# Performance work log

Measured on AMD Instinct MI355X. Metric: run time of the kernel, lower is better.

Reference implementation:

```python
import jax, jax.numpy as jnp
import numpy as np

G = 8192          # graphs per hand side (PyG batch)
J_SRC = 17        # source-hand joints (transform: Linear(17*64, 13*64))
J_TGT = 13        # target-hand joints
NEG_SLOPE = 0.01  # F.leaky_relu default


def _chain_edge_index(J, num_graphs):
    # bidirectional chain tree per graph, block-diagonal batched like PyG
    p = np.arange(J - 1); c = np.arange(1, J)
    src = np.concatenate([p, c]); dst = np.concatenate([c, p])
    base = np.arange(num_graphs)[:, None] * J
    return jnp.asarray(np.stack([(src[None] + base).ravel(), (dst[None] + base).ravel()]), jnp.int32)


def _lin_init(key, o, i):
    k1, k2 = jax.random.split(key)
    s = 1.0 / np.sqrt(i)
    return (jax.random.uniform(k1, (o, i), jnp.float32, -s, s),
            jax.random.uniform(k2, (o,), jnp.float32, -s, s))


def setup_inputs() -> dict:
    key = jax.random.key(0)
    ks = iter(jax.random.split(key, 64))
    inp = {}
    Nl = G * J_SRC
    inp["l_hand_x"] = jax.random.normal(next(ks), (Nl, 3), jnp.float32)
    inp["r_hand_x"] = jax.random.normal(next(ks), (Nl, 3), jnp.float32)
    ei_src = _chain_edge_index(J_SRC, G)
    inp["l_hand_edge_index"] = ei_src
    inp["r_hand_edge_index"] = ei_src
    E_src = ei_src.shape[1]
    inp["l_hand_edge_attr"] = jax.random.normal(next(ks), (E_src, 3), jnp.float32)
    inp["r_hand_edge_attr"] = jax.random.normal(next(ks), (E_src, 3), jnp.float32)
    ei_t = _chain_edge_index(J_TGT, G)
    inp["hand_edge_index"] = ei_t
    inp["hand_edge_attr"] = jax.random.normal(next(ks), (ei_t.shape[1], 6), jnp.float32)
    Nt = G * J_TGT
    inp["hand_lower"] = -(jax.random.uniform(next(ks), (Nt, 1), jnp.float32) + 0.5)
    inp["hand_upper"] = jax.random.uniform(next(ks), (Nt, 1), jnp.float32) + 0.5
    inp["hand_offset"] = jax.random.normal(next(ks), (Nt, 3), jnp.float32) * 0.05
    ax = jax.random.normal(next(ks), (Nt, 3), jnp.float32)
    inp["hand_axis"] = ax / jnp.linalg.norm(ax, axis=-1, keepdims=True)
    par = np.concatenate([[-1], np.arange(J_TGT - 1)])  # chain: root then parents
    inp["hand_parent"] = jnp.asarray(np.tile(par, G), jnp.int32)
    inp["num_graphs"] = G
    dims = {"enc1_lin": (16, 9),  "enc1_up": (16, 3),
            "enc2_lin": (32, 35), "enc2_up": (32, 16),
            "enc3_lin": (64, 67), "enc3_up": (64, 32),
            "trans":    (13 * 64, 17 * 64),
            "dec1_lin": (32, 138), "dec1_up": (32, 66),
            "dec2_lin": (16, 70),  "dec2_up": (16, 32),
            "dec3_lin": (1, 38),   "dec3_up": (1, 16)}
    for n, (o, i) in dims.items():
        W, b = _lin_init(next(ks), o, i)
        inp[n + "_W"] = W; inp[n + "_b"] = b
    return inp


def _block(x, ei, ea, Wl, bl, Wu, bu):
    # SpatialBasicBlock: gather x_i/x_j, concat edge_attr, linear+leaky_relu,
    # scatter-add at target nodes, residual upsample of x.
    src, dst = ei[0], ei[1]
    z = jnp.concatenate([x[dst], x[src], ea], axis=-1)  # [E, 2*in+edge]
    m = jax.nn.leaky_relu(z @ Wl.T + bl, NEG_SLOPE)
    agg = jax.ops.segment_sum(m, dst, num_segments=x.shape[0])
    return agg + x @ Wu.T + bu


def _rodrigues(ax, ang):
    # rotation matrices about unit axis ax [...,3] by angle ang [...]
    c = jnp.cos(ang)[..., None, None]; s = jnp.sin(ang)[..., None, None]
    I = jnp.eye(3, dtype=ax.dtype)
    aa = ax[..., :, None] * ax[..., None, :]
    x, y, z = ax[..., 0], ax[..., 1], ax[..., 2]
    zero = jnp.zeros_like(x)
    K = jnp.stack([jnp.stack([zero, -z, y], -1),
                   jnp.stack([z, zero, -x], -1),
                   jnp.stack([-y, x, zero], -1)], -2)
    return c * I + (1 - c) * aa + s * K


def _fk(ang, parent, offset, axis, num_graphs, J):
    # forward kinematics along parent chain (parent[j] < j, root = -1)
    a = ang.reshape(num_graphs, J)
    off = offset.reshape(num_graphs, J, 3)
    ax = axis.reshape(num_graphs, J, 3)
    par = parent.reshape(num_graphs, J)[0]  # same topology in every graph
    Rl = _rodrigues(ax, a)                  # [G, J, 3, 3] local rotations
    I = jnp.eye(3, dtype=ang.dtype)
    pos = jnp.zeros((num_graphs, J, 3), ang.dtype)
    rot = jnp.zeros((num_graphs, J, 3, 3), ang.dtype)
    for j in range(J):  # J=13 fixed structural loop
        p = par[j]
        root = p < 0
        Rp = jnp.where(root, I, jnp.take(rot, p, axis=1))
        Pp = jnp.where(root, 0.0, jnp.take(pos, p, axis=1))
        pos = pos.at[:, j].set(Pp + jnp.einsum('gab,gb->ga', Rp, off[:, j]))
        rot = rot.at[:, j].set(jnp.einsum('gab,gbc->gac', Rp, Rl[:, j]))
    return pos.reshape(-1, 3)


def reference(l_hand_x, r_hand_x, l_hand_edge_index, r_hand_edge_index,
              l_hand_edge_attr, r_hand_edge_attr, hand_edge_index, hand_edge_attr,
              hand_lower, hand_upper, hand_offset, hand_axis, hand_parent, num_graphs,
              enc1_lin_W, enc1_lin_b, enc1_up_W, enc1_up_b,
              enc2_lin_W, enc2_lin_b, enc2_up_W, enc2_up_b,
              enc3_lin_W, enc3_lin_b, enc3_up_W, enc3_up_b,
              trans_W, trans_b,
              dec1_lin_W, dec1_lin_b, dec1_up_W, dec1_up_b,
              dec2_lin_W, dec2_lin_b, dec2_up_W, dec2_up_b,
              dec3_lin_W, dec3_lin_b, dec3_up_W, dec3_up_b):
    # ---- encode ----
    Nl = l_hand_x.shape[0]
    x = jnp.concatenate([l_hand_x, r_hand_x], axis=0)
    ei = jnp.concatenate([l_hand_edge_index, r_hand_edge_index + Nl], axis=1)
    ea = jnp.concatenate([l_hand_edge_attr, r_hand_edge_attr], axis=0)
    h = _block(x, ei, ea, enc1_lin_W, enc1_lin_b, enc1_up_W, enc1_up_b)
    h = _block(h, ei, ea, enc2_lin_W, enc2_lin_b, enc2_up_W, enc2_up_b)
    h = _block(h, ei, ea, enc3_lin_W, enc3_lin_b, enc3_up_W, enc3_up_b)
    G2 = 2 * num_graphs
    z = jnp.tanh(h.reshape(G2, -1) @ trans_W.T + trans_b).reshape(-1, 64)
    # ---- decode ----
    half = z.shape[0] // 2
    ei_t = jnp.concatenate([hand_edge_index, hand_edge_index + half], axis=1)
    ea_t = jnp.concatenate([hand_edge_attr, hand_edge_attr], axis=0)
    lower = jnp.concatenate([hand_lower, hand_lower], axis=0)
    upper = jnp.concatenate([hand_upper, hand_upper], axis=0)
    offset = jnp.concatenate([hand_offset, hand_offset], axis=0)
    axis = jnp.concatenate([hand_axis, hand_axis], axis=0)
    parent = jnp.concatenate([hand_parent, hand_parent], axis=0)
    xd = jnp.concatenate([z, lower, upper], axis=1)  # [2*G*13, 66]
    h = _block(xd, ei_t, ea_t, dec1_lin_W, dec1_lin_b, dec1_up_W, dec1_up_b)
    h = _block(h, ei_t, ea_t, dec2_lin_W, dec2_lin_b, dec2_up_W, dec2_up_b)
    ang = jnp.tanh(_block(h, ei_t, ea_t, dec3_lin_W, dec3_lin_b, dec3_up_W, dec3_up_b))
    ang = lower + (upper - lower) * (ang + 1) / 2
    pos = _fk(ang, parent, offset, axis, G2, J_TGT)
    hn = ang.shape[0] // 2
    return ang[:hn], pos[:hn], ang[hn:], pos[hn:]
```

## Files before the change

### kernel.cpp

```cpp
#include <hip/hip_runtime.h>
#include <math.h>


constexpr int G_NUM = 8192;
constexpr int JS = 17;
constexpr int JT = 13;
constexpr int N_ENC = 2 * G_NUM * JS;
constexpr int N_DEC = 2 * G_NUM * JT;
constexpr int G2 = 2 * G_NUM;
constexpr int HN = G_NUM * JT;
constexpr int K_TR = JS * 64;
constexpr int N_TR = JT * 64;

typedef unsigned short u16;
typedef u16   u16x8 __attribute__((ext_vector_type(8)));
typedef u16   u16x4 __attribute__((ext_vector_type(4)));
typedef float f32x4 __attribute__((ext_vector_type(4)));
typedef __bf16 bf16x8 __attribute__((ext_vector_type(8)));

__device__ __forceinline__ float lrelu(float v) { return v > 0.f ? v : 0.01f * v; }
__device__ __forceinline__ u16 f2bf(float f) {
    unsigned u = __float_as_uint(f);
    u += 0x7fff + ((u >> 16) & 1);
    return (u16)(u >> 16);
}
__device__ __forceinline__ float bf2f(u16 h) { return __uint_as_float((unsigned)h << 16); }

template<int K_MM, int C_IN_W, int C_OUT, int C_E, int J, int G, bool TAIL>
__global__ __launch_bounds__(256)
void block_mfma(const u16* __restrict__ xHi, const u16* __restrict__ xLo,
                const float* __restrict__ eaA, const float* __restrict__ eaB, int g_half,
                const float* __restrict__ lowv, const float* __restrict__ upv,
                const float* __restrict__ Wl, const float* __restrict__ bl,
                const float* __restrict__ Wu, const float* __restrict__ bu,
                u16* __restrict__ outHi, u16* __restrict__ outLo)
{
    constexpr int ROWS = G * J;
    constexpr int F = (ROWS + 15) / 16;
    constexpr int NCH = C_OUT / 16;
    constexpr int KF = K_MM / 32;
    constexpr int KPAD = K_MM + 8;
    constexpr int EAS = 2 * (J - 1) * C_E;
    constexpr int CTOT = 2 * C_IN_W + C_E;
    constexpr int CW = (C_IN_W < K_MM) ? C_IN_W : K_MM;
    constexpr int WGG = 4 * G;

    __shared__ __align__(16) u16 sWH[3 * C_OUT * KPAD], sWL[3 * C_OUT * KPAD];
    __shared__ float sEA[WGG * EAS];
    __shared__ float sWe[C_OUT * C_E];
    __shared__ float sBl[C_OUT], sBu[C_OUT];
    __shared__ float sTl[TAIL ? 6 * C_OUT : 1];
    __shared__ float sLow[TAIL ? WGG * J : 1], sUpp[TAIL ? WGG * J : 1];

    const int t = threadIdx.x;
    const int g0 = blockIdx.x * WGG;

    for (int i = t; i < 3 * C_OUT * K_MM; i += 256) {
        const int ch = i / K_MM, k = i % K_MM;
        const int p = ch / C_OUT, o = ch % C_OUT;
        float v = 0.f;
        if (k < CW) {
            if (p == 0)      v = Wl[o * CTOT + k];
            else if (p == 1) v = Wl[o * CTOT + C_IN_W + k];
            else             v = Wu[o * C_IN_W + k];
        }
        const u16 h = f2bf(v);
        sWH[ch * KPAD + k] = h;
        sWL[ch * KPAD + k] = f2bf(v - bf2f(h));
    }
    for (int i = t; i < WGG * EAS; i += 256) {
        const int lg = i / EAS, r = i % EAS;
        const int g = g0 + lg;
        sEA[i] = (g < g_half) ? eaA[(size_t)g * EAS + r]
                              : eaB[(size_t)(g - g_half) * EAS + r];
    }
    for (int i = t; i < C_OUT * C_E; i += 256)
        sWe[i] = Wl[(i / C_E) * CTOT + 2 * C_IN_W + (i % C_E)];
    if (t < C_OUT) { sBl[t] = bl[t]; sBu[t] = bu[t]; }
    if constexpr (TAIL) {
        if (t < C_OUT) {
            sTl[t * 6 + 0] = Wl[t * CTOT + K_MM];
            sTl[t * 6 + 1] = Wl[t * CTOT + K_MM + 1];
            sTl[t * 6 + 2] = Wl[t * CTOT + C_IN_W + K_MM];
            sTl[t * 6 + 3] = Wl[t * CTOT + C_IN_W + K_MM + 1];
            sTl[t * 6 + 4] = Wu[t * C_IN_W + K_MM];
            sTl[t * 6 + 5] = Wu[t * C_IN_W + K_MM + 1];
        }
        for (int i = t; i < WGG * J; i += 256) {
            const int lg = i / J, j = i % J;
            const int g = g0 + lg;
            const int ge = (g < g_half) ? g : g - g_half;
            sLow[i] = lowv[ge * J + j];
            sUpp[i] = upv[ge * J + j];
        }
    }
    __syncthreads();

    const int wv = t >> 6, lane = t & 63;
    const int col = lane & 15, kg = lane >> 4;
    const size_t baseNode = (size_t)(blockIdx.x * 4 + wv) * ROWS;
    const int lgB = wv * G;

    for (int ch = 0; ch < NCH; ++ch) {
        const int o = ch * 16 + col;
        bf16x8 wUh[KF], wUl[KF], wVh[KF], wVl[KF], wPh[KF], wPl[KF];
        #pragma unroll
        for (int kf = 0; kf < KF; ++kf) {
            wUh[kf] = *(const bf16x8*)&sWH[(0 * C_OUT + o) * KPAD + kf * 32 + kg * 8];
            wUl[kf] = *(const bf16x8*)&sWL[(0 * C_OUT + o) * KPAD + kf * 32 + kg * 8];
            wVh[kf] = *(const bf16x8*)&sWH[(1 * C_OUT + o) * KPAD + kf * 32 + kg * 8];
            wVl[kf] = *(const bf16x8*)&sWL[(1 * C_OUT + o) * KPAD + kf * 32 + kg * 8];
            wPh[kf] = *(const bf16x8*)&sWH[(2 * C_OUT + o) * KPAD + kf * 32 + kg * 8];
            wPl[kf] = *(const bf16x8*)&sWL[(2 * C_OUT + o) * KPAD + kf * 32 + kg * 8];
        }
        float we[C_E];
        #pragma unroll
        for (int k = 0; k < C_E; ++k) we[k] = sWe[o * C_E + k];
        const float blo = sBl[o], buo = sBu[o];
        float tl0 = 0, tl1 = 0, tl2 = 0, tl3 = 0, tl4 = 0, tl5 = 0;
        if constexpr (TAIL) {
            tl0 = sTl[o * 6 + 0]; tl1 = sTl[o * 6 + 1]; tl2 = sTl[o * 6 + 2];
            tl3 = sTl[o * 6 + 3]; tl4 = sTl[o * 6 + 4]; tl5 = sTl[o * 6 + 5];
        }

        f32x4 Vpp = {0,0,0,0}, Vp = {0,0,0,0};
        f32x4 Up = {0,0,0,0}, Pp = {0,0,0,0};
        #pragma unroll
        for (int f = 0; f <= F; ++f) {
            f32x4 Vc = {0,0,0,0}, Uc = {0,0,0,0}, Pc = {0,0,0,0};
            if (f < F) {
                const int nrow = f * 16 + col;
                const size_t nd = baseNode + (nrow < ROWS ? nrow : ROWS - 1);
                #pragma unroll
                for (int kf = 0; kf < KF; ++kf) {
                    const bf16x8 aH = *(const bf16x8*)&xHi[nd * K_MM + kf * 32 + kg * 8];
                    const bf16x8 aL = *(const bf16x8*)&xLo[nd * K_MM + kf * 32 + kg * 8];
                    Vc = __builtin_amdgcn_mfma_f32_16x16x32_bf16(aH, wVh[kf], Vc, 0, 0, 0);
                    Vc = __builtin_amdgcn_mfma_f32_16x16x32_bf16(aH, wVl[kf], Vc, 0, 0, 0);
                    Vc = __builtin_amdgcn_mfma_f32_16x16x32_bf16(aL, wVh[kf], Vc, 0, 0, 0);
                    Uc = __builtin_amdgcn_mfma_f32_16x16x32_bf16(aH, wUh[kf], Uc, 0, 0, 0);
                    Uc = __builtin_amdgcn_mfma_f32_16x16x32_bf16(aH, wUl[kf], Uc, 0, 0, 0);
                    Uc = __builtin_amdgcn_mfma_f32_16x16x32_bf16(aL, wUh[kf], Uc, 0, 0, 0);
                    Pc = __builtin_amdgcn_mfma_f32_16x16x32_bf16(aH, wPh[kf], Pc, 0, 0, 0);
                    Pc = __builtin_amdgcn_mfma_f32_16x16x32_bf16(aH, wPl[kf], Pc, 0, 0, 0);
                    Pc = __builtin_amdgcn_mfma_f32_16x16x32_bf16(aL, wPh[kf], Pc, 0, 0, 0);
                }
            }
            if (f >= 1) {
                const int fm = f - 1;
                const float vL0a = __shfl(Vpp[3], 48 + col);
                const float vL0b = __shfl(Vp[3], (lane - 16) & 63);
                const float vL0 = (kg == 0) ? vL0a : vL0b;
                const float vR3a = __shfl(Vc[0], col);
                const float vR3b = __shfl(Vp[0], (lane + 16) & 63);
                const float vR3 = (kg == 3) ? vR3a : vR3b;
                #pragma unroll
                for (int r = 0; r < 4; ++r) {
                    const int row = fm * 16 + kg * 4 + r;
                    const bool valid = row < ROWS;
                    const int jpos = row % J;
                    int gl = row / J; if (gl > G - 1) gl = G - 1;
                    const int lg = lgB + gl;
                    const bool h1m = valid && (jpos > 0);
                    const bool h2m = valid && (jpos < J - 1);
                    const int jm = jpos > 0 ? jpos - 1 : 0;
                    float e1 = 0.f, e2 = 0.f;
                    #pragma unroll
                    for (int k = 0; k < C_E; ++k) {
                        e1 = fmaf(we[k], sEA[lg * EAS + jm * C_E + k], e1);
                        e2 = fmaf(we[k], sEA[lg * EAS + (J - 1 + jpos) * C_E + k], e2);
                    }
                    float vL = (r == 0) ? vL0 : Vp[r - 1];
                    float vR = (r == 3) ? vR3 : Vp[r + 1];
                    float u = Up[r], p = Pp[r];
                    if constexpr (TAIL) {
                        const int jp = jpos < J - 1 ? jpos + 1 : J - 1;
                        u = fmaf(tl0, sLow[lg * J + jpos], u);
                        u = fmaf(tl1, sUpp[lg * J + jpos], u);
                        p = fmaf(tl4, sLow[lg * J + jpos], p);
                        p = fmaf(tl5, sUpp[lg * J + jpos], p);
                        vL = fmaf(tl2, sLow[lg * J + jm], vL);
                        vL = fmaf(tl3, sUpp[lg * J + jm], vL);
                        vR = fmaf(tl2, sLow[lg * J + jp], vR);
                        vR = fmaf(tl3, sUpp[lg * J + jp], vR);
                    }
                    const float m1 = u + vL + e1 + blo;
                    const float m2 = u + vR + e2 + blo;
                    const float res = p + buo + (h1m ? lrelu(m1) : 0.f) + (h2m ? lrelu(m2) : 0.f);
                    if (valid) {
                        const size_t node = baseNode + row;
                        const u16 hh = f2bf(res);
                        outHi[node * C_OUT + o] = hh;
                        outLo[node * C_OUT + o] = f2bf(res - bf2f(hh));
                    }
                }
            }
            Vpp = Vp; Vp = Vc; Up = Uc; Pp = Pc;
        }
    }
}

template<int C_IN, int C_OUT, int C_E, int J, int NN, int OPAD>
__global__ __launch_bounds__(256)
void block_small(const float* __restrict__ xA, const float* __restrict__ xB, int node_half,
                 const float* __restrict__ eaA, const float* __restrict__ eaB, int g_half,
                 const float* __restrict__ Wl, const float* __restrict__ bl,
                 const float* __restrict__ Wu, const float* __restrict__ bu,
                 u16* __restrict__ outHi, u16* __restrict__ outLo, int N)
{
    constexpr int CTOT = 2 * C_IN + C_E;
    constexpr int SOP = C_OUT + 1;
    constexpr int NPB = 256 / C_OUT;
    __shared__ float wl_T[CTOT * SOP];
    __shared__ float wu_T[C_IN * SOP];
    __shared__ float bl_s[C_OUT], bu_s[C_OUT];
    const int t = threadIdx.x;
    for (int i = t; i < C_OUT * CTOT; i += 256) { int oo = i / CTOT, kk = i % CTOT; wl_T[kk * SOP + oo] = Wl[i]; }
    for (int i = t; i < C_OUT * C_IN; i += 256) { int oo = i / C_IN, kk = i % C_IN; wu_T[kk * SOP + oo] = Wu[i]; }
    if (t < C_OUT) { bl_s[t] = bl[t]; bu_s[t] = bu[t]; }
    __syncthreads();

    const int o = t % C_OUT;
    const int s = t / C_OUT;
    const int nb = (blockIdx.x * NPB + s) * NN;
    float up[NN], m1[NN], m2[NN];
    #pragma unroll
    for (int i = 0; i < NN; ++i) { up[i] = bu_s[o]; m1[i] = bl_s[o]; m2[i] = bl_s[o]; }
    auto clampn = [&](int nd) { return nd < 0 ? 0 : (nd >= N ? N - 1 : nd); };

    for (int k = 0; k < C_IN; ++k) {
        const float w0 = wl_T[k * SOP + o];
        const float w1 = wl_T[(C_IN + k) * SOP + o];
        const float wuv = wu_T[k * SOP + o];
        float xs[NN + 2];
        #pragma unroll
        for (int i = 0; i < NN + 2; ++i) {
            const int nd = clampn(nb - 1 + i);
            xs[i] = (nd < node_half) ? xA[(size_t)nd * C_IN + k]
                                     : xB[(size_t)(nd - node_half) * C_IN + k];
        }
        #pragma unroll
        for (int nd = 0; nd < NN; ++nd) {
            up[nd] = fmaf(wuv, xs[nd + 1], up[nd]);
            m1[nd] = fmaf(w0, xs[nd + 1], m1[nd]);
            m1[nd] = fmaf(w1, xs[nd], m1[nd]);
            m2[nd] = fmaf(w0, xs[nd + 1], m2[nd]);
            m2[nd] = fmaf(w1, xs[nd + 2], m2[nd]);
        }
    }
    #pragma unroll
    for (int nd = 0; nd < NN; ++nd) {
        const int node = nb + nd;
        const int g = node / J;
        const int j = node - g * J;
        const bool has1 = (j > 0), has2 = (j < J - 1);
        const int geff = (g < g_half) ? g : g - g_half;
        const float* ea = (g < g_half) ? eaA : eaB;
        const ptrdiff_t e1 = ((ptrdiff_t)geff * 2 * (J - 1) + (j - 1)) * C_E;
        const ptrdiff_t e2 = ((ptrdiff_t)geff * 2 * (J - 1) + (J - 1) + j) * C_E;
        float a1 = m1[nd], a2 = m2[nd];
        #pragma unroll
        for (int k = 0; k < C_E; ++k) {
            const float w = wl_T[(2 * C_IN + k) * SOP + o];
            if (has1) a1 = fmaf(w, ea[e1 + k], a1);
            if (has2) a2 = fmaf(w, ea[e2 + k], a2);
        }
        const float v = up[nd] + (has1 ? lrelu(a1) : 0.f) + (has2 ? lrelu(a2) : 0.f);
        const u16 hh = f2bf(v);
        outHi[(size_t)node * OPAD + o] = hh;
        outLo[(size_t)node * OPAD + o] = f2bf(v - bf2f(hh));
        if (OPAD > C_OUT) {
            outHi[(size_t)node * OPAD + o + C_OUT] = 0;
            outLo[(size_t)node * OPAD + o + C_OUT] = 0;
        }
    }
}

__global__ __launch_bounds__(256)
void trans_mfma(const u16* __restrict__ aHi, const u16* __restrict__ aLo,
                const float* __restrict__ W, const float* __restrict__ bias,
                u16* __restrict__ zHi, u16* __restrict__ zLo)
{
    constexpr int NI = K_TR / 32;
    constexpr int ST = 40;
    __shared__ __align__(16) u16 sAH[128 * ST], sAL[128 * ST];
    __shared__ __align__(16) u16 sBH[128 * ST], sBL[128 * ST];
    const int t = threadIdx.x, lane = t & 63, w = t >> 6;
    const int wm = w >> 1, wn = w & 1, lr = lane & 15, kg = lane >> 4;
    const int bm = blockIdx.x * 128, bn = blockIdx.y * 128;
    const int sr = t >> 1, sc = (t & 1) * 16;

    u16x8 rA[4];
    float4 rW[4];
    auto gload = [&](int i) {
        const int k0 = i * 32;
        const size_t oa = (size_t)(bm + sr) * K_TR + k0 + sc;
        rA[0] = *(const u16x8*)&aHi[oa];
        rA[1] = *(const u16x8*)&aHi[oa + 8];
        rA[2] = *(const u16x8*)&aLo[oa];
        rA[3] = *(const u16x8*)&aLo[oa + 8];
        int wrow = bn + sr; if (wrow > N_TR - 1) wrow = N_TR - 1;
        const size_t ow = (size_t)wrow * K_TR + k0 + sc;
        rW[0] = *(const float4*)&W[ow];
        rW[1] = *(const float4*)&W[ow + 4];
        rW[2] = *(const float4*)&W[ow + 8];
        rW[3] = *(const float4*)&W[ow + 12];
    };
    auto stage = [&]() {
        *(u16x8*)&sAH[sr * ST + sc]     = rA[0];
        *(u16x8*)&sAH[sr * ST + sc + 8] = rA[1];
        *(u16x8*)&sAL[sr * ST + sc]     = rA[2];
        *(u16x8*)&sAL[sr * ST + sc + 8] = rA[3];
        const float fv[16] = {rW[0].x, rW[0].y, rW[0].z, rW[0].w,
                              rW[1].x, rW[1].y, rW[1].z, rW[1].w,
                              rW[2].x, rW[2].y, rW[2].z, rW[2].w,
                              rW[3].x, rW[3].y, rW[3].z, rW[3].w};
        u16x8 hq0, lq0, hq1, lq1;
        #pragma unroll
        for (int j = 0; j < 8; ++j) {
            const __bf16 hb0 = (__bf16)fv[j];
            const __bf16 lb0 = (__bf16)(fv[j] - (float)hb0);
            hq0[j] = __builtin_bit_cast(u16, hb0);
            lq0[j] = __builtin_bit_cast(u16, lb0);
            const __bf16 hb1 = (__bf16)fv[8 + j];
            const __bf16 lb1 = (__bf16)(fv[8 + j] - (float)hb1);
            hq1[j] = __builtin_bit_cast(u16, hb1);
            lq1[j] = __builtin_bit_cast(u16, lb1);
        }
        *(u16x8*)&sBH[sr * ST + sc]     = hq0;
        *(u16x8*)&sBH[sr * ST + sc + 8] = hq1;
        *(u16x8*)&sBL[sr * ST + sc]     = lq0;
        *(u16x8*)&sBL[sr * ST + sc + 8] = lq1;
    };

    f32x4 acc[4][4];
    #pragma unroll
    for (int m = 0; m < 4; ++m)
        #pragma unroll
        for (int n = 0; n < 4; ++n) acc[m][n] = f32x4{0.f, 0.f, 0.f, 0.f};

    auto step = [&]() {
        bf16x8 ah[4], al[4], bh[4], bl2[4];
        #pragma unroll
        for (int m = 0; m < 4; ++m) {
            const int r = wm * 64 + m * 16 + lr;
            ah[m] = *(const bf16x8*)&sAH[r * ST + kg * 8];
            al[m] = *(const bf16x8*)&sAL[r * ST + kg * 8];
        }
        #pragma unroll
        for (int n = 0; n < 4; ++n) {
            const int r = wn * 64 + n * 16 + lr;
            bh[n]  = *(const bf16x8*)&sBH[r * ST + kg * 8];
            bl2[n] = *(const bf16x8*)&sBL[r * ST + kg * 8];
        }
        #pragma unroll
        for (int m = 0; m < 4; ++m)
            #pragma unroll
            for (int n = 0; n < 4; ++n) {
                acc[m][n] = __builtin_amdgcn_mfma_f32_16x16x32_bf16(ah[m], bh[n],  acc[m][n], 0, 0, 0);
                acc[m][n] = __builtin_amdgcn_mfma_f32_16x16x32_bf16(ah[m], bl2[n], acc[m][n], 0, 0, 0);
                acc[m][n] = __builtin_amdgcn_mfma_f32_16x16x32_bf16(al[m], bh[n],  acc[m][n], 0, 0, 0);
            }
    };

    gload(0);
    stage();
    __syncthreads();
    for (int i = 0; i < NI; ++i) {
        if (i + 1 < NI) gload(i + 1);
        step();
        __syncthreads();
        if (i + 1 < NI) stage();
        __syncthreads();
    }

    #pragma unroll
    for (int n = 0; n < 4; ++n) {
        const int colz = bn + wn * 64 + n * 16 + lr;
        if (colz < N_TR) {
            const float bv = bias[colz];
            #pragma unroll
            for (int m = 0; m < 4; ++m)
                #pragma unroll
                for (int r = 0; r < 4; ++r) {
                    const int row = bm + wm * 64 + m * 16 + kg * 4 + r;
                    const float v = tanhf(acc[m][n][r] + bv);
                    const size_t idx = (size_t)row * N_TR + colz;
                    const u16 hh = f2bf(v);
                    zHi[idx] = hh;
                    zLo[idx] = f2bf(v - bf2f(hh));
                }
        }
    }
}

__global__ __launch_bounds__(256)
void dec3fk_kernel(const u16* __restrict__ xHi, const u16* __restrict__ xLo,
                   const float* __restrict__ ea,
                   const float* __restrict__ Wl, const float* __restrict__ bl,
                   const float* __restrict__ Wu, const float* __restrict__ bu,
                   const float* __restrict__ lowv, const float* __restrict__ upv,
                   const float* __restrict__ offset, const float* __restrict__ axis,
                   float* __restrict__ dout)
{
    const int g2 = blockIdx.x * 256 + threadIdx.x;
    if (g2 >= G2) return;
    const int geff = (g2 >= G_NUM) ? g2 - G_NUM : g2;
    const bool rightH = (g2 >= G_NUM);

    auto loadrow = [&](int nd, float* x) {
        const u16x8 h0 = *(const u16x8*)&xHi[(size_t)nd * 16];
        const u16x8 h1 = *(const u16x8*)&xHi[(size_t)nd * 16 + 8];
        const u16x8 l0 = *(const u16x8*)&xLo[(size_t)nd * 16];
        const u16x8 l1 = *(const u16x8*)&xLo[(size_t)nd * 16 + 8];
        #pragma unroll
        for (int k = 0; k < 8; ++k) {
            x[k]     = bf2f(h0[k]) + bf2f(l0[k]);
            x[k + 8] = bf2f(h1[k]) + bf2f(l1[k]);
        }
    };

    float xprev[16], xcur[16], xnext[16];
    #pragma unroll
    for (int k = 0; k < 16; ++k) xprev[k] = 0.f;
    loadrow(g2 * JT, xcur);
    loadrow(g2 * JT + 1, xnext);

    float R[9];
    float px = 0.f, py = 0.f, pz = 0.f;
    for (int j = 0; j < JT; ++j) {
        const int node = g2 * JT + j;
        const bool has1 = (j > 0), has2 = (j < JT - 1);
        float m1 = bl[0], m2 = m1, up = bu[0];
        #pragma unroll
        for (int k = 0; k < 16; ++k) {
            const float xd = xcur[k];
            up = fmaf(Wu[k], xd, up);
            const float w0 = Wl[k];
            m1 = fmaf(w0, xd, m1);
            m2 = fmaf(w0, xd, m2);
            const float w1 = Wl[16 + k];
            m1 = fmaf(w1, xprev[k], m1);
            m2 = fmaf(w1, xnext[k], m2);
        }
        const int e1 = (geff * 24 + (j - 1)) * 6;
        const int e2 = (geff * 24 + 12 + j) * 6;
        #pragma unroll
        for (int k = 0; k < 6; ++k) {
            const float ww = Wl[32 + k];
            if (has1) m1 = fmaf(ww, ea[e1 + k], m1);
            if (has2) m2 = fmaf(ww, ea[e2 + k], m2);
        }
        const float v = up + (has1 ? lrelu(m1) : 0.f) + (has2 ? lrelu(m2) : 0.f);
        const int idx = geff * JT + j;
        const float lo = lowv[idx], hi = upv[idx];
        const float a = lo + (hi - lo) * (tanhf(v) + 1.f) * 0.5f;
        if (!rightH) dout[node] = a;
        else         dout[4 * HN + idx] = a;

        const float ax = axis[idx * 3], ay = axis[idx * 3 + 1], az = axis[idx * 3 + 2];
        const float ox = offset[idx * 3], oy = offset[idx * 3 + 1], oz = offset[idx * 3 + 2];
        const float c = cosf(a), s = sinf(a), ic = 1.f - c;
        const float L[9] = {
            c + ic * ax * ax,      ic * ax * ay - s * az, ic * ax * az + s * ay,
            ic * ay * ax + s * az, c + ic * ay * ay,      ic * ay * az - s * ax,
            ic * az * ax - s * ay, ic * az * ay + s * ax, c + ic * az * az };
        if (j == 0) {
            px = ox; py = oy; pz = oz;
            #pragma unroll
            for (int q = 0; q < 9; ++q) R[q] = L[q];
        } else {
            px += R[0] * ox + R[1] * oy + R[2] * oz;
            py += R[3] * ox + R[4] * oy + R[5] * oz;
            pz += R[6] * ox + R[7] * oy + R[8] * oz;
            float T[9];
            #pragma unroll
            for (int r = 0; r < 3; ++r)
                #pragma unroll
                for (int cc = 0; cc < 3; ++cc)
                    T[r * 3 + cc] = R[r * 3] * L[cc] + R[r * 3 + 1] * L[3 + cc] + R[r * 3 + 2] * L[6 + cc];
            #pragma unroll
            for (int q = 0; q < 9; ++q) R[q] = T[q];
        }
        const int pbase = (!rightH) ? (HN + node * 3) : (5 * HN + idx * 3);
        dout[pbase] = px; dout[pbase + 1] = py; dout[pbase + 2] = pz;

        #pragma unroll
        for (int k = 0; k < 16; ++k) { xprev[k] = xcur[k]; xcur[k] = xnext[k]; }
        const int nn = node + 2 < N_DEC ? node + 2 : N_DEC - 1;
        if (j < JT - 1) loadrow(nn, xnext);
    }
}

extern "C" void kernel_launch(void* const* d_in, const int* in_sizes, int n_in,
                              void* d_out, int out_size, void* d_ws, size_t ws_size,
                              hipStream_t stream)
{
    const float* l_x  = (const float*)d_in[0];
    const float* r_x  = (const float*)d_in[1];
    const float* l_ea = (const float*)d_in[4];
    const float* r_ea = (const float*)d_in[5];
    const float* ea_t = (const float*)d_in[7];
    const float* lowv = (const float*)d_in[8];
    const float* upv  = (const float*)d_in[9];
    const float* offs = (const float*)d_in[10];
    const float* axis = (const float*)d_in[11];
    const float* e1lW = (const float*)d_in[14]; const float* e1lB = (const float*)d_in[15];
    const float* e1uW = (const float*)d_in[16]; const float* e1uB = (const float*)d_in[17];
    const float* e2lW = (const float*)d_in[18]; const float* e2lB = (const float*)d_in[19];
    const float* e2uW = (const float*)d_in[20]; const float* e2uB = (const float*)d_in[21];
    const float* e3lW = (const float*)d_in[22]; const float* e3lB = (const float*)d_in[23];
    const float* e3uW = (const float*)d_in[24]; const float* e3uB = (const float*)d_in[25];
    const float* trW  = (const float*)d_in[26]; const float* trB  = (const float*)d_in[27];
    const float* d1lW = (const float*)d_in[28]; const float* d1lB = (const float*)d_in[29];
    const float* d1uW = (const float*)d_in[30]; const float* d1uB = (const float*)d_in[31];
    const float* d2lW = (const float*)d_in[32]; const float* d2lB = (const float*)d_in[33];
    const float* d2uW = (const float*)d_in[34]; const float* d2uB = (const float*)d_in[35];
    const float* d3lW = (const float*)d_in[36]; const float* d3lB = (const float*)d_in[37];
    const float* d3uW = (const float*)d_in[38]; const float* d3uB = (const float*)d_in[39];

    char* ws = (char*)d_ws;
    u16* h1H  = (u16*)(ws + 0);          u16* h1L  = (u16*)(ws + 17825792);
    u16* h2H  = (u16*)(ws + 71303168);   u16* h2L  = (u16*)(ws + 89128960);
    u16* aH   = (u16*)(ws + 0);          u16* aL   = (u16*)(ws + 35651584);
    u16* zzH  = (u16*)(ws + 71303168);   u16* zzL  = (u16*)(ws + 98566144);
    u16* hd1H = (u16*)(ws + 0);          u16* hd1L = (u16*)(ws + 13631488);
    u16* hd2H = (u16*)(ws + 27262976);   u16* hd2L = (u16*)(ws + 34078720);
    float* outp = (float*)d_out;

    block_small<3, 16, 3, JS, 4, 32><<<N_ENC / 64, 256, 0, stream>>>(
        l_x, r_x, G_NUM * JS, l_ea, r_ea, G_NUM,
        e1lW, e1lB, e1uW, e1uB, h1H, h1L, N_ENC);
    block_mfma<32, 16, 32, 3, JS, 4, false><<<1024, 256, 0, stream>>>(
        h1H, h1L, l_ea, r_ea, G_NUM, nullptr, nullptr,
        e2lW, e2lB, e2uW, e2uB, h2H, h2L);
    block_mfma<32, 32, 64, 3, JS, 4, false><<<1024, 256, 0, stream>>>(
        h2H, h2L, l_ea, r_ea, G_NUM, nullptr, nullptr,
        e3lW, e3lB, e3uW, e3uB, aH, aL);
    trans_mfma<<<dim3(G2 / 128, (N_TR + 127) / 128), 256, 0, stream>>>(
        aH, aL, trW, trB, zzH, zzL);
    block_mfma<64, 66, 32, 6, JT, 4, true><<<1024, 256, 0, stream>>>(
        zzH, zzL, ea_t, ea_t, G_NUM, lowv, upv,
        d1lW, d1lB, d1uW, d1uB, hd1H, hd1L);
    block_mfma<32, 32, 16, 6, JT, 4, false><<<1024, 256, 0, stream>>>(
        hd1H, hd1L, ea_t, ea_t, G_NUM, nullptr, nullptr,
        d2lW, d2lB, d2uW, d2uB, hd2H, hd2L);
    dec3fk_kernel<<<(G2 + 255) / 256, 256, 0, stream>>>(
        hd2H, hd2L, ea_t, d3lW, d3lB, d3uW, d3uB, lowv, upv, offs, axis, outp);
}
```

Baseline: 531.7 us.

## Stage transform A-tiles via global_load_lds and restructure block kernels per channel group

The transform GEMM now moves activation tiles directly from global memory into LDS using global_load_lds, which removes the register round-trip and the padded LDS layout. The weight tile is still converted to hi/lo bf16 through registers. A new block_mfma2 kernel keeps the weights for several output-channel groups in registers and loops over row fragments. The encoder-3 launch splits its channels across a 2-D grid and decoder-1 runs with one block per graph group. This is meant to raise MFMA work per x load and cut staging overhead, but the unpadded LDS layout may cause bank conflicts and holding more register weights may lower occupancy.

```diff
diff --git a/kernel.cpp b/kernel.cpp
--- a/kernel.cpp
+++ b/kernel.cpp
@@ -14,7 +14,6 @@
 
 typedef unsigned short u16;
 typedef u16   u16x8 __attribute__((ext_vector_type(8)));
-typedef u16   u16x4 __attribute__((ext_vector_type(4)));
 typedef float f32x4 __attribute__((ext_vector_type(4)));
 typedef __bf16 bf16x8 __attribute__((ext_vector_type(8)));
 
@@ -25,6 +24,11 @@
     return (u16)(u >> 16);
 }
 __device__ __forceinline__ float bf2f(u16 h) { return __uint_as_float((unsigned)h << 16); }
+__device__ __forceinline__ void gld16(const void* g, void* l) {
+    __builtin_amdgcn_global_load_lds(
+        (const __attribute__((address_space(1))) unsigned int*)g,
+        (__attribute__((address_space(3))) unsigned int*)l, 16, 0, 0);
+}
 
 template<int K_MM, int C_IN_W, int C_OUT, int C_E, int J, int G, bool TAIL>
 __global__ __launch_bounds__(256)
@@ -200,6 +204,197 @@
     }
 }
 
+template<int K_MM, int C_IN_W, int C_OUT, int C_E, int J, int G, bool TAIL, int NCHB>
+__global__ __launch_bounds__(256)
+void block_mfma2(const u16* __restrict__ xHi, const u16* __restrict__ xLo,
+                 const float* __restrict__ eaA, const float* __restrict__ eaB, int g_half,
+                 const float* __restrict__ lowv, const float* __restrict__ upv,
+                 const float* __restrict__ Wl, const float* __restrict__ bl,
+                 const float* __restrict__ Wu, const float* __restrict__ bu,
+                 u16* __restrict__ outHi, u16* __restrict__ outLo)
+{
+    constexpr int ROWS = G * J;
+    constexpr int F = (ROWS + 15) / 16;
+    constexpr int KF = K_MM / 32;
+    constexpr int KPAD = K_MM + 8;
+    constexpr int EAS = 2 * (J - 1) * C_E;
+    constexpr int CTOT = 2 * C_IN_W + C_E;
+    constexpr int CW = (C_IN_W < K_MM) ? C_IN_W : K_MM;
+    constexpr int WGG = 4 * G;
+
+    __shared__ __align__(16) u16 sWH[3 * C_OUT * KPAD], sWL[3 * C_OUT * KPAD];
+    __shared__ float sEA[WGG * EAS];
+    __shared__ float sWe[C_OUT * C_E];
+    __shared__ float sBl[C_OUT], sBu[C_OUT];
+    __shared__ float sTl[TAIL ? 6 * C_OUT : 1];
+    __shared__ float sLow[TAIL ? WGG * J : 1], sUpp[TAIL ? WGG * J : 1];
+
+    const int t = threadIdx.x;
+    const int g0 = blockIdx.x * WGG;
+
+    for (int i = t; i < 3 * C_OUT * K_MM; i += 256) {
+        const int ch = i / K_MM, k = i % K_MM;
+        const int p = ch / C_OUT, o = ch % C_OUT;
+        float v = 0.f;
+        if (k < CW) {
+            if (p == 0)      v = Wl[o * CTOT + k];
+            else if (p == 1) v = Wl[o * CTOT + C_IN_W + k];
+            else             v = Wu[o * C_IN_W + k];
+        }
+        const u16 h = f2bf(v);
+        sWH[ch * KPAD + k] = h;
+        sWL[ch * KPAD + k] = f2bf(v - bf2f(h));
+    }
+    for (int i = t; i < WGG * EAS; i += 256) {
+        const int lg = i / EAS, r = i % EAS;
+        const int g = g0 + lg;
+        sEA[i] = (g < g_half) ? eaA[(size_t)g * EAS + r]
+                              : eaB[(size_t)(g - g_half) * EAS + r];
+    }
+    for (int i = t; i < C_OUT * C_E; i += 256)
+        sWe[i] = Wl[(i / C_E) * CTOT + 2 * C_IN_W + (i % C_E)];
+    if (t < C_OUT) { sBl[t] = bl[t]; sBu[t] = bu[t]; }
+    if constexpr (TAIL) {
+        if (t < C_OUT) {
+            sTl[t * 6 + 0] = Wl[t * CTOT + K_MM];
+            sTl[t * 6 + 1] = Wl[t * CTOT + K_MM + 1];
+            sTl[t * 6 + 2] = Wl[t * CTOT + C_IN_W + K_MM];
+            sTl[t * 6 + 3] = Wl[t * CTOT + C_IN_W + K_MM + 1];
+            sTl[t * 6 + 4] = Wu[t * C_IN_W + K_MM];
+            sTl[t * 6 + 5] = Wu[t * C_IN_W + K_MM + 1];
+        }
+        for (int i = t; i < WGG * J; i += 256) {
+            const int lg = i / J, j = i % J;
+            const int g = g0 + lg;
+            const int ge = (g < g_half) ? g : g - g_half;
+            sLow[i] = lowv[ge * J + j];
+            sUpp[i] = upv[ge * J + j];
+        }
+    }
+    __syncthreads();
+
+    const int wv = t >> 6, lane = t & 63;
+    const int col = lane & 15, kg = lane >> 4;
+    const size_t baseNode = (size_t)(blockIdx.x * 4 + wv) * ROWS;
+    const int lgB = wv * G;
+    const int chBase = blockIdx.y * NCHB;
+
+    bf16x8 wUh[NCHB][KF], wUl[NCHB][KF], wVh[NCHB][KF], wVl[NCHB][KF], wPh[NCHB][KF], wPl[NCHB][KF];
+    float we[NCHB][C_E];
+    float blo[NCHB], buo[NCHB];
+    float tl0[NCHB], tl1[NCHB], tl2[NCHB], tl3[NCHB], tl4[NCHB], tl5[NCHB];
+    #pragma unroll
+    for (int q = 0; q < NCHB; ++q) {
+        const int o = (chBase + q) * 16 + col;
+        #pragma unroll
+        for (int kf = 0; kf < KF; ++kf) {
+            wUh[q][kf] = *(const bf16x8*)&sWH[(0 * C_OUT + o) * KPAD + kf * 32 + kg * 8];
+            wUl[q][kf] = *(const bf16x8*)&sWL[(0 * C_OUT + o) * KPAD + kf * 32 + kg * 8];
+            wVh[q][kf] = *(const bf16x8*)&sWH[(1 * C_OUT + o) * KPAD + kf * 32 + kg * 8];
+            wVl[q][kf] = *(const bf16x8*)&sWL[(1 * C_OUT + o) * KPAD + kf * 32 + kg * 8];
+            wPh[q][kf] = *(const bf16x8*)&sWH[(2 * C_OUT + o) * KPAD + kf * 32 + kg * 8];
+            wPl[q][kf] = *(const bf16x8*)&sWL[(2 * C_OUT + o) * KPAD + kf * 32 + kg * 8];
+        }
+        #pragma unroll
+        for (int k = 0; k < C_E; ++k) we[q][k] = sWe[o * C_E + k];
+        blo[q] = sBl[o]; buo[q] = sBu[o];
+        tl0[q] = tl1[q] = tl2[q] = tl3[q] = tl4[q] = tl5[q] = 0.f;
+        if constexpr (TAIL) {
+            tl0[q] = sTl[o * 6 + 0]; tl1[q] = sTl[o * 6 + 1]; tl2[q] = sTl[o * 6 + 2];
+            tl3[q] = sTl[o * 6 + 3]; tl4[q] = sTl[o * 6 + 4]; tl5[q] = sTl[o * 6 + 5];
+        }
+    }
+
+    f32x4 Vp[NCHB], Up[NCHB], Pp[NCHB];
+    float vLast[NCHB];
+    #pragma unroll
+    for (int q = 0; q < NCHB; ++q) { Vp[q] = f32x4{0,0,0,0}; Up[q] = Vp[q]; Pp[q] = Vp[q]; vLast[q] = 0.f; }
+
+    #pragma unroll
+    for (int f = 0; f <= F; ++f) {
+        bf16x8 aH[KF], aL[KF];
+        const bool haveX = f < F;
+        if (haveX) {
+            const int nrow = f * 16 + col;
+            const size_t nd = baseNode + (nrow < ROWS ? nrow : ROWS - 1);
+            #pragma unroll
+            for (int kf = 0; kf < KF; ++kf) {
+                aH[kf] = *(const bf16x8*)&xHi[nd * K_MM + kf * 32 + kg * 8];
+                aL[kf] = *(const bf16x8*)&xLo[nd * K_MM + kf * 32 + kg * 8];
+            }
+        }
+        #pragma unroll
+        for (int q = 0; q < NCHB; ++q) {
+            f32x4 Vc = {0,0,0,0}, Uc = {0,0,0,0}, Pc = {0,0,0,0};
+            if (haveX) {
+                #pragma unroll
+                for (int kf = 0; kf < KF; ++kf) {
+                    Vc = __builtin_amdgcn_mfma_f32_16x16x32_bf16(aH[kf], wVh[q][kf], Vc, 0, 0, 0);
+                    Vc = __builtin_amdgcn_mfma_f32_16x16x32_bf16(aH[kf], wVl[q][kf], Vc, 0, 0, 0);
+                    Vc = __builtin_amdgcn_mfma_f32_16x16x32_bf16(aL[kf], wVh[q][kf], Vc, 0, 0, 0);
+                    Uc = __builtin_amdgcn_mfma_f32_16x16x32_bf16(aH[kf], wUh[q][kf], Uc, 0, 0, 0);
+                    Uc = __builtin_amdgcn_mfma_f32_16x16x32_bf16(aH[kf], wUl[q][kf], Uc, 0, 0, 0);
+                    Uc = __builtin_amdgcn_mfma_f32_16x16x32_bf16(aL[kf], wUh[q][kf], Uc, 0, 0, 0);
+                    Pc = __builtin_amdgcn_mfma_f32_16x16x32_bf16(aH[kf], wPh[q][kf], Pc, 0, 0, 0);
+                    Pc = __builtin_amdgcn_mfma_f32_16x16x32_bf16(aH[kf], wPl[q][kf], Pc, 0, 0, 0);
+                    Pc = __builtin_amdgcn_mfma_f32_16x16x32_bf16(aL[kf], wPh[q][kf], Pc, 0, 0, 0);
+                }
+            }
+            if (f >= 1) {
+                const int fm = f - 1;
+                const float vL0b = __shfl(Vp[q][3], (lane - 16) & 63);
+                const float vL0 = (kg == 0) ? vLast[q] : vL0b;
+                const float vR3a = __shfl(Vc[0], col);
+                const float vR3b = __shfl(Vp[q][0], (lane + 16) & 63);
+                const float vR3 = (kg == 3) ? vR3a : vR3b;
+                #pragma unroll
+                for (int r = 0; r < 4; ++r) {
+                    const int row = fm * 16 + kg * 4 + r;
+                    const bool valid = row < ROWS;
+                    const int jpos = row % J;
+                    int gl = row / J; if (gl > G - 1) gl = G - 1;
+                    const int lg = lgB + gl;
+                    const bool h1m = valid && (jpos > 0);
+                    const bool h2m = valid && (jpos < J - 1);
+                    const int jm = jpos > 0 ? jpos - 1 : 0;
+                    float e1 = 0.f, e2 = 0.f;
+                    #pragma unroll
+                    for (int k = 0; k < C_E; ++k) {
+                        e1 = fmaf(we[q][k], sEA[lg * EAS + jm * C_E + k], e1);
+                        e2 = fmaf(we[q][k], sEA[lg * EAS + (J - 1 + jpos) * C_E + k], e2);
+                    }
+                    float vL = (r == 0) ? vL0 : Vp[q][r - 1];
+                    float vR = (r == 3) ? vR3 : Vp[q][r + 1];
+                    float u = Up[q][r], p = Pp[q][r];
+                    if constexpr (TAIL) {
+                        const int jp = jpos < J - 1 ? jpos + 1 : J - 1;
+                        u = fmaf(tl0[q], sLow[lg * J + jpos], u);
+                        u = fmaf(tl1[q], sUpp[lg * J + jpos], u);
+                        p = fmaf(tl4[q], sLow[lg * J + jpos], p);
+                        p = fmaf(tl5[q], sUpp[lg * J + jpos], p);
+                        vL = fmaf(tl2[q], sLow[lg * J + jm], vL);
+                        vL = fmaf(tl3[q], sUpp[lg * J + jm], vL);
+                        vR = fmaf(tl2[q], sLow[lg * J + jp], vR);
+                        vR = fmaf(tl3[q], sUpp[lg * J + jp], vR);
+                    }
+                    const float m1 = u + vL + e1 + blo[q];
+                    const float m2 = u + vR + e2 + blo[q];
+                    const float res = p + buo[q] + (h1m ? lrelu(m1) : 0.f) + (h2m ? lrelu(m2) : 0.f);
+                    if (valid) {
+                        const size_t node = baseNode + row;
+                        const int o = (chBase + q) * 16 + col;
+                        const u16 hh = f2bf(res);
+                        outHi[node * C_OUT + o] = hh;
+                        outLo[node * C_OUT + o] = f2bf(res - bf2f(hh));
+                    }
+                }
+            }
+            vLast[q] = __shfl(Vp[q][3], 48 + col);
+            Vp[q] = Vc; Up[q] = Uc; Pp[q] = Pc;
+        }
+    }
+}
+
 template<int C_IN, int C_OUT, int C_E, int J, int NN, int OPAD>
 __global__ __launch_bounds__(256)
 void block_small(const float* __restrict__ xA, const float* __restrict__ xB, int node_half,
@@ -282,55 +477,52 @@
                 u16* __restrict__ zHi, u16* __restrict__ zLo)
 {
     constexpr int NI = K_TR / 32;
-    constexpr int ST = 40;
-    __shared__ __align__(16) u16 sAH[128 * ST], sAL[128 * ST];
-    __shared__ __align__(16) u16 sBH[128 * ST], sBL[128 * ST];
+    __shared__ __align__(16) u16 sAH[128 * 32], sAL[128 * 32];
+    __shared__ __align__(16) u16 sBH[128 * 32], sBL[128 * 32];
     const int t = threadIdx.x, lane = t & 63, w = t >> 6;
     const int wm = w >> 1, wn = w & 1, lr = lane & 15, kg = lane >> 4;
     const int bm = blockIdx.x * 128, bn = blockIdx.y * 128;
-    const int sr = t >> 1, sc = (t & 1) * 16;
-
-    u16x8 rA[4];
+
+    auto aload = [&](int i) {
+        const int k0 = i * 32;
+        #pragma unroll
+        for (int c = 0; c < 2; ++c) {
+            const int p = c * 256 + t;
+            const size_t oa = (size_t)(bm + (p >> 2)) * K_TR + k0 + (p & 3) * 8;
+            const int ldsbase = (c * 256 + w * 64) * 8;
+            gld16(&aHi[oa], &sAH[ldsbase]);
+            gld16(&aLo[oa], &sAL[ldsbase]);
+        }
+    };
     float4 rW[4];
-    auto gload = [&](int i) {
+    auto wload = [&](int i) {
         const int k0 = i * 32;
-        const size_t oa = (size_t)(bm + sr) * K_TR + k0 + sc;
-        rA[0] = *(const u16x8*)&aHi[oa];
-        rA[1] = *(const u16x8*)&aHi[oa + 8];
-        rA[2] = *(const u16x8*)&aLo[oa];
-        rA[3] = *(const u16x8*)&aLo[oa + 8];
-        int wrow = bn + sr; if (wrow > N_TR - 1) wrow = N_TR - 1;
-        const size_t ow = (size_t)wrow * K_TR + k0 + sc;
-        rW[0] = *(const float4*)&W[ow];
-        rW[1] = *(const float4*)&W[ow + 4];
-        rW[2] = *(const float4*)&W[ow + 8];
-        rW[3] = *(const float4*)&W[ow + 12];
+        #pragma unroll
+        for (int c = 0; c < 2; ++c) {
+            const int p = c * 256 + t;
+            int wrow = bn + (p >> 2); if (wrow > N_TR - 1) wrow = N_TR - 1;
+            const size_t ow = (size_t)wrow * K_TR + k0 + (p & 3) * 8;
+            rW[2 * c]     = *(const float4*)&W[ow];
+            rW[2 * c + 1] = *(const float4*)&W[ow + 4];
+        }
     };
-    auto stage = [&]() {
-        *(u16x8*)&sAH[sr * ST + sc]     = rA[0];
-        *(u16x8*)&sAH[sr * ST + sc + 8] = rA[1];
-        *(u16x8*)&sAL[sr * ST + sc]     = rA[2];
-        *(u16x8*)&sAL[sr * ST + sc + 8] = rA[3];
-        const float fv[16] = {rW[0].x, rW[0].y, rW[0].z, rW[0].w,
-                              rW[1].x, rW[1].y, rW[1].z, rW[1].w,
-                              rW[2].x, rW[2].y, rW[2].z, rW[2].w,
-                              rW[3].x, rW[3].y, rW[3].z, rW[3].w};
-        u16x8 hq0, lq0, hq1, lq1;
-        #pragma unroll
-        for (int j = 0; j < 8; ++j) {
-            const __bf16 hb0 = (__bf16)fv[j];
-            const __bf16 lb0 = (__bf16)(fv[j] - (float)hb0);
-            hq0[j] = __builtin_bit_cast(u16, hb0);
-            lq0[j] = __builtin_bit_cast(u16, lb0);
-            const __bf16 hb1 = (__bf16)fv[8 + j];
-            const __bf16 lb1 = (__bf16)(fv[8 + j] - (float)hb1);
-            hq1[j] = __builtin_bit_cast(u16, hb1);
-            lq1[j] = __builtin_bit_cast(u16, lb1);
-        }
-        *(u16x8*)&sBH[sr * ST + sc]     = hq0;
-        *(u16x8*)&sBH[sr * ST + sc + 8] = hq1;
-        *(u16x8*)&sBL[sr * ST + sc]     = lq0;
-        *(u16x8*)&sBL[sr * ST + sc + 8] = lq1;
+    auto wstore = [&]() {
+        #pragma unroll
+        for (int c = 0; c < 2; ++c) {
+            const int p = c * 256 + t;
+            const float fv[8] = {rW[2*c].x, rW[2*c].y, rW[2*c].z, rW[2*c].w,
+                                 rW[2*c+1].x, rW[2*c+1].y, rW[2*c+1].z, rW[2*c+1].w};
+            u16x8 hq, lq;
+            #pragma unroll
+            for (int j = 0; j < 8; ++j) {
+                const __bf16 hb = (__bf16)fv[j];
+                const __bf16 lb = (__bf16)(fv[j] - (float)hb);
+                hq[j] = __builtin_bit_cast(u16, hb);
+                lq[j] = __builtin_bit_cast(u16, lb);
+            }
+            *(u16x8*)&sBH[p * 8] = hq;
+            *(u16x8*)&sBL[p * 8] = lq;
+        }
     };
 
     f32x4 acc[4][4];
@@ -344,14 +536,14 @@
         #pragma unroll
         for (int m = 0; m < 4; ++m) {
             const int r = wm * 64 + m * 16 + lr;
-            ah[m] = *(const bf16x8*)&sAH[r * ST + kg * 8];
-            al[m] = *(const bf16x8*)&sAL[r * ST + kg * 8];
+            ah[m] = *(const bf16x8*)&sAH[r * 32 + kg * 8];
+            al[m] = *(const bf16x8*)&sAL[r * 32 + kg * 8];
         }
         #pragma unroll
         for (int n = 0; n < 4; ++n) {
             const int r = wn * 64 + n * 16 + lr;
-            bh[n]  = *(const bf16x8*)&sBH[r * ST + kg * 8];
-            bl2[n] = *(const bf16x8*)&sBL[r * ST + kg * 8];
+            bh[n]  = *(const bf16x8*)&sBH[r * 32 + kg * 8];
+            bl2[n] = *(const bf16x8*)&sBL[r * 32 + kg * 8];
         }
         #pragma unroll
         for (int m = 0; m < 4; ++m)
@@ -363,14 +555,15 @@
             }
     };
 
-    gload(0);
-    stage();
+    wload(0);
+    aload(0);
+    wstore();
     __syncthreads();
     for (int i = 0; i < NI; ++i) {
-        if (i + 1 < NI) gload(i + 1);
+        if (i + 1 < NI) wload(i + 1);
         step();
         __syncthreads();
-        if (i + 1 < NI) stage();
+        if (i + 1 < NI) { aload(i + 1); wstore(); }
         __syncthreads();
     }
 
@@ -534,12 +727,12 @@
     block_mfma<32, 16, 32, 3, JS, 4, false><<<1024, 256, 0, stream>>>(
         h1H, h1L, l_ea, r_ea, G_NUM, nullptr, nullptr,
         e2lW, e2lB, e2uW, e2uB, h2H, h2L);
-    block_mfma<32, 32, 64, 3, JS, 4, false><<<1024, 256, 0, stream>>>(
+    block_mfma2<32, 32, 64, 3, JS, 4, false, 2><<<dim3(1024, 2), 256, 0, stream>>>(
         h2H, h2L, l_ea, r_ea, G_NUM, nullptr, nullptr,
         e3lW, e3lB, e3uW, e3uB, aH, aL);
     trans_mfma<<<dim3(G2 / 128, (N_TR + 127) / 128), 256, 0, stream>>>(
         aH, aL, trW, trB, zzH, zzL);
-    block_mfma<64, 66, 32, 6, JT, 4, true><<<1024, 256, 0, stream>>>(
+    block_mfma2<64, 66, 32, 6, JT, 4, true, 2><<<dim3(1024, 1), 256, 0, stream>>>(
         zzH, zzL, ea_t, ea_t, G_NUM, lowv, upv,
         d1lW, d1lB, d1uW, d1uB, hd1H, hd1L);
     block_mfma<32, 32, 16, 6, JT, 4, false><<<1024, 256, 0, stream>>>(
```

Result: no change. 537.7 us (+1.1%).
